# Kernel tuning notes

Hardware: AMD Instinct MI355X
Metric: run time of the kernel (lower is better)

Reference implementation:

```python
import jax, jax.numpy as jnp
import numpy as np

LEVEL = 3
NDIM = 2 ** LEVEL  # 8 quantized dims
SCALE = 0.9990000128746033


def setup_inputs() -> dict:
    key = jax.random.key(0)
    k1, k2, k3 = jax.random.split(key, 3)
    B, T, D = 8, 8192, 1280
    x = jax.random.normal(k1, (B, T, D), dtype=jnp.float32)
    # nn.Linear(D, 8): weight (8, D), bias (8)
    W = jax.random.normal(k2, (NDIM, D), dtype=jnp.float32) / np.sqrt(D)
    b = jax.random.normal(k3, (NDIM,), dtype=jnp.float32) * 0.01
    return {"x": x, "W": W, "b": b}


def reference(x, W, b):
    B, T, D = x.shape
    xf = x.reshape(-1, D)                       # (B*T, D)
    h = jnp.einsum('nd,kd->nk', xf, W) + b      # (B*T, 8) skinny GEMM
    h = jnp.tanh(h.astype(jnp.float32)) * SCALE
    h = jnp.round(h) + 1.0                      # ternary {0,1,2}
    powers = jnp.power(jnp.float32(LEVEL), jnp.arange(NDIM, dtype=jnp.float32))
    mu = jnp.sum(h * powers, axis=-1)           # base-3 index as float
    return mu.reshape(B, T).astype(jnp.int32)
```

## Files before the change

kernel.cpp:

```cpp
#include <hip/hip_runtime.h>
#include <math.h>

#define DIM 1280
#define NDIM 8
#define CHUNKS 5

__global__ __launch_bounds__(256, 2)
void fsq_kernel(const float* __restrict__ x, const float* __restrict__ W,
                const float* __restrict__ b, int* __restrict__ out, int n_tok) {
    const int lane    = threadIdx.x & 63;
    const int wave    = (int)((blockIdx.x * blockDim.x + threadIdx.x) >> 6);
    const int n_waves = (int)((gridDim.x * blockDim.x) >> 6);

    const float T = (float)atanh(0.5 / 0.9990000128746033);

    float4 w[CHUNKS][NDIM];
    #pragma unroll
    for (int c = 0; c < CHUNKS; ++c) {
        #pragma unroll
        for (int k = 0; k < NDIM; ++k) {
            w[c][k] = *(const float4*)(W + k * DIM + c * 256 + lane * 4);
        }
    }

    float bias[NDIM];
    #pragma unroll
    for (int k = 0; k < NDIM; ++k) bias[k] = b[k];

    for (int t = wave; t < n_tok; t += n_waves) {
        const float4* xp = (const float4*)(x + (size_t)t * DIM);
        float4 xv[CHUNKS];
        #pragma unroll
        for (int c = 0; c < CHUNKS; ++c) xv[c] = xp[c * 64 + lane];

        float acc[NDIM];
        #pragma unroll
        for (int k = 0; k < NDIM; ++k) acc[k] = 0.0f;

        #pragma unroll
        for (int c = 0; c < CHUNKS; ++c) {
            #pragma unroll
            for (int k = 0; k < NDIM; ++k) {
                acc[k] = fmaf(xv[c].x, w[c][k].x, acc[k]);
                acc[k] = fmaf(xv[c].y, w[c][k].y, acc[k]);
                acc[k] = fmaf(xv[c].z, w[c][k].z, acc[k]);
                acc[k] = fmaf(xv[c].w, w[c][k].w, acc[k]);
            }
        }

        #pragma unroll
        for (int k = 0; k < NDIM; ++k) {
            #pragma unroll
            for (int off = 32; off >= 1; off >>= 1) {
                acc[k] += __shfl_xor(acc[k], off, 64);
            }
        }

        int mu = 0, p3 = 1;
        #pragma unroll
        for (int k = 0; k < NDIM; ++k) {
            float h = acc[k] + bias[k];
            int d = 1 + (h > T ? 1 : 0) - (h < -T ? 1 : 0);
            mu += d * p3;
            p3 *= 3;
        }
        if (lane == 0) out[t] = mu;
    }
}

extern "C" void kernel_launch(void* const* d_in, const int* in_sizes, int n_in,
                              void* d_out, int out_size, void* d_ws, size_t ws_size,
                              hipStream_t stream) {
    const float* x = (const float*)d_in[0];
    const float* W = (const float*)d_in[1];
    const float* b = (const float*)d_in[2];
    int* out = (int*)d_out;

    const int n_tok = in_sizes[0] / DIM;
    const int blocks = 2048;
    fsq_kernel<<<blocks, 256, 0, stream>>>(x, W, b, out, n_tok);
}
```

Before: 442.9 us.

## Double-buffer token loads and use transpose-style butterfly reduction across 8 outputs

```diff
diff --git a/kernel.cpp b/kernel.cpp
--- a/kernel.cpp
+++ b/kernel.cpp
@@ -4,6 +4,66 @@
 #define DIM 1280
 #define NDIM 8
 #define CHUNKS 5
+
+__device__ __forceinline__ void load_x(const float* __restrict__ x, int t, int lane,
+                                       float4 xv[CHUNKS]) {
+    const float4* xp = (const float4*)(x + (size_t)t * DIM);
+    #pragma unroll
+    for (int c = 0; c < CHUNKS; ++c) xv[c] = xp[c * 64 + lane];
+}
+
+__device__ __forceinline__ void compute_store(const float4 xv[CHUNKS],
+                                              const float4 w[CHUNKS][NDIM],
+                                              float T, float bd, int p3,
+                                              int lane, int t, int* __restrict__ out) {
+    float acc[NDIM];
+    #pragma unroll
+    for (int k = 0; k < NDIM; ++k) acc[k] = 0.0f;
+
+    #pragma unroll
+    for (int c = 0; c < CHUNKS; ++c) {
+        #pragma unroll
+        for (int k = 0; k < NDIM; ++k) {
+            acc[k] = fmaf(xv[c].x, w[c][k].x, acc[k]);
+            acc[k] = fmaf(xv[c].y, w[c][k].y, acc[k]);
+            acc[k] = fmaf(xv[c].z, w[c][k].z, acc[k]);
+            acc[k] = fmaf(xv[c].w, w[c][k].w, acc[k]);
+        }
+    }
+
+    const int bit0 = lane & 1, bit1 = lane & 2, bit2 = lane & 4;
+    float r4[4];
+    #pragma unroll
+    for (int j = 0; j < 4; ++j) {
+        float send = bit0 ? acc[j] : acc[j + 4];
+        float recv = __shfl_xor(send, 1, 64);
+        r4[j] = (bit0 ? acc[j + 4] : acc[j]) + recv;
+    }
+    float r2[2];
+    #pragma unroll
+    for (int j = 0; j < 2; ++j) {
+        float send = bit1 ? r4[j] : r4[j + 2];
+        float recv = __shfl_xor(send, 2, 64);
+        r2[j] = (bit1 ? r4[j + 2] : r4[j]) + recv;
+    }
+    float r1;
+    {
+        float send = bit2 ? r2[0] : r2[1];
+        float recv = __shfl_xor(send, 4, 64);
+        r1 = (bit2 ? r2[1] : r2[0]) + recv;
+    }
+    r1 += __shfl_xor(r1, 8, 64);
+    r1 += __shfl_xor(r1, 16, 64);
+    r1 += __shfl_xor(r1, 32, 64);
+
+    float h = r1 + bd;
+    int dig = 1 + (h > T ? 1 : 0) - (h < -T ? 1 : 0);
+    int mu = dig * p3;
+    mu += __shfl_xor(mu, 1, 64);
+    mu += __shfl_xor(mu, 2, 64);
+    mu += __shfl_xor(mu, 4, 64);
+    if (lane == 0) out[t] = mu;
+}
 
 __global__ __launch_bounds__(256, 2)
 void fsq_kernel(const float* __restrict__ x, const float* __restrict__ W,
@@ -14,6 +74,11 @@
 
     const float T = (float)atanh(0.5 / 0.9990000128746033);
 
+    const int d = ((lane & 1) << 2) | (lane & 2) | ((lane >> 2) & 1);
+    const float bd = b[d];
+    int p3 = 1;
+    for (int i = 0; i < d; ++i) p3 *= 3;
+
     float4 w[CHUNKS][NDIM];
     #pragma unroll
     for (int c = 0; c < CHUNKS; ++c) {
@@ -23,48 +88,22 @@
         }
     }
 
-    float bias[NDIM];
-    #pragma unroll
-    for (int k = 0; k < NDIM; ++k) bias[k] = b[k];
+    int t = wave;
+    if (t >= n_tok) return;
 
-    for (int t = wave; t < n_tok; t += n_waves) {
-        const float4* xp = (const float4*)(x + (size_t)t * DIM);
-        float4 xv[CHUNKS];
-        #pragma unroll
-        for (int c = 0; c < CHUNKS; ++c) xv[c] = xp[c * 64 + lane];
+    float4 xa[CHUNKS], xb[CHUNKS];
+    load_x(x, t, lane, xa);
+    while (true) {
+        const int t1 = t + n_waves;
+        if (t1 < n_tok) load_x(x, t1, lane, xb);
+        compute_store(xa, w, T, bd, p3, lane, t, out);
+        if (t1 >= n_tok) break;
 
-        float acc[NDIM];
-        #pragma unroll
-        for (int k = 0; k < NDIM; ++k) acc[k] = 0.0f;
-
-        #pragma unroll
-        for (int c = 0; c < CHUNKS; ++c) {
-            #pragma unroll
-            for (int k = 0; k < NDIM; ++k) {
-                acc[k] = fmaf(xv[c].x, w[c][k].x, acc[k]);
-                acc[k] = fmaf(xv[c].y, w[c][k].y, acc[k]);
-                acc[k] = fmaf(xv[c].z, w[c][k].z, acc[k]);
-                acc[k] = fmaf(xv[c].w, w[c][k].w, acc[k]);
-            }
-        }
-
-        #pragma unroll
-        for (int k = 0; k < NDIM; ++k) {
-            #pragma unroll
-            for (int off = 32; off >= 1; off >>= 1) {
-                acc[k] += __shfl_xor(acc[k], off, 64);
-            }
-        }
-
-        int mu = 0, p3 = 1;
-        #pragma unroll
-        for (int k = 0; k < NDIM; ++k) {
-            float h = acc[k] + bias[k];
-            int d = 1 + (h > T ? 1 : 0) - (h < -T ? 1 : 0);
-            mu += d * p3;
-            p3 *= 3;
-        }
-        if (lane == 0) out[t] = mu;
+        const int t2 = t1 + n_waves;
+        if (t2 < n_tok) load_x(x, t2, lane, xa);
+        compute_store(xb, w, T, bd, p3, lane, t1, out);
+        if (t2 >= n_tok) break;
+        t = t2;
     }
 }
 
```

After: 445.4 us. About the same (+0.6%).
